# Kernel tuning notes

Hardware: AMD Instinct MI355X
Metric: run time of the kernel (lower is better)

## Reference

```python
import jax, jax.numpy as jnp
import numpy as np

N = 100000   # nodes
E = 1600000  # edges (avg degree 16)
F = 128      # input features
H = 64       # hidden_dim
C = 10       # num_classes
G = 128      # graphs in batch
EPS = 1e-5   # BatchNorm eps


def setup_inputs() -> dict:
    key = jax.random.key(0)
    ks = jax.random.split(key, 24)
    d = {}
    d['x'] = jax.random.normal(ks[0], (N, F), jnp.float32)
    d['edge_index'] = jax.random.randint(ks[1], (2, E), 0, N)
    d['batch'] = jnp.sort(jax.random.randint(ks[2], (N,), 0, G))
    # SAGEConv1: lin_l (aggregated, with bias) + lin_r (root, no bias)
    d['W1l'] = jax.random.normal(ks[3], (F, H), jnp.float32) * 0.05
    d['W1r'] = jax.random.normal(ks[4], (F, H), jnp.float32) * 0.05
    d['b1'] = jnp.zeros((H,), jnp.float32)
    # SAGEConv2
    d['W2l'] = jax.random.normal(ks[5], (H, H), jnp.float32) * 0.1
    d['W2r'] = jax.random.normal(ks[6], (H, H), jnp.float32) * 0.1
    d['b2'] = jnp.zeros((H,), jnp.float32)
    # BatchNorm (eval mode: running stats)
    for i, (kg, kb, km, kv) in enumerate([(7, 8, 9, 10), (11, 12, 13, 14), (15, 16, 17, 18)], 1):
        d[f'bn{i}_g'] = jax.random.uniform(ks[kg], (H,), jnp.float32, 0.5, 1.5)
        d[f'bn{i}_b'] = jax.random.normal(ks[kb], (H,), jnp.float32) * 0.1
        d[f'bn{i}_m'] = jax.random.normal(ks[km], (H,), jnp.float32) * 0.1
        d[f'bn{i}_v'] = jax.random.uniform(ks[kv], (H,), jnp.float32, 0.5, 1.5)
    # classifier head
    d['Wc1'] = jax.random.normal(ks[19], (H, H), jnp.float32) * 0.1
    d['bc1'] = jnp.zeros((H,), jnp.float32)
    d['Wc2'] = jax.random.normal(ks[20], (H, C), jnp.float32) * 0.1
    d['bc2'] = jnp.zeros((C,), jnp.float32)
    return d


def _bn(x, g, b, m, v):
    return (x - m) * jax.lax.rsqrt(v + EPS) * g + b


def _sage(x, src, dst, Wl, Wr, b):
    # mean aggregation of source-node features at destination nodes
    msum = jax.ops.segment_sum(x[src], dst, num_segments=N)          # [N, d]
    cnt = jax.ops.segment_sum(jnp.ones((E,), x.dtype), dst, num_segments=N)
    mean = msum / jnp.maximum(cnt, 1.0)[:, None]
    return mean @ Wl + b + x @ Wr


def reference(x, edge_index, batch,
              W1l, W1r, b1, W2l, W2r, b2,
              bn1_g, bn1_b, bn1_m, bn1_v,
              bn2_g, bn2_b, bn2_m, bn2_v,
              Wc1, bc1, bn3_g, bn3_b, bn3_m, bn3_v,
              Wc2, bc2):
    src, dst = edge_index[0], edge_index[1]
    h = _sage(x, src, dst, W1l, W1r, b1)
    h = jax.nn.relu(_bn(h, bn1_g, bn1_b, bn1_m, bn1_v))
    h = _sage(h, src, dst, W2l, W2r, b2)
    h = jax.nn.relu(_bn(h, bn2_g, bn2_b, bn2_m, bn2_v))
    # global mean pool over graphs
    gsum = jax.ops.segment_sum(h, batch, num_segments=G)             # [G, H]
    gcnt = jax.ops.segment_sum(jnp.ones((N,), h.dtype), batch, num_segments=G)
    g = gsum / jnp.maximum(gcnt, 1.0)[:, None]
    # classifier head (eval: dropout is identity)
    g = jax.nn.relu(_bn(g @ Wc1 + bc1, bn3_g, bn3_b, bn3_m, bn3_v))
    logits = g @ Wc2 + bc2
    return jax.nn.log_softmax(logits, axis=1)
```

## Files before the change

kernel.cpp:

```cpp
#include <hip/hip_runtime.h>
#include <hip/hip_bf16.h>
#include <math.h>

#define NN 100000
#define NE 1600000
#define FF 128
#define HH 64
#define CC 10
#define GG 128
#define BN_EPS 1e-5f

#define BNODES 64
#define NB 1563
#define PBLK 256
#define ECHUNK 6250
#define SCOL_CAP 2048

#define PNODES 16
#define POOL_BLOCKS 1563

typedef short v8bf __attribute__((ext_vector_type(8)));
typedef float v4f  __attribute__((ext_vector_type(4)));

__device__ inline ushort f2b(float x) {
    __hip_bfloat16 h = __float2bfloat16(x);
    return *reinterpret_cast<ushort*>(&h);
}
__device__ inline float b2f(ushort u) {
    return __uint_as_float(((unsigned)u) << 16);
}
__device__ inline float blo(unsigned u) { return __uint_as_float(u << 16); }
__device__ inline float bhi(unsigned u) { return __uint_as_float(u & 0xffff0000u); }

__device__ inline void sw_one(const float* __restrict__ W, ushort* __restrict__ o,
                              int t, int K) {
    const int lane = t & 63, nt = (t >> 6) & 3, ks = t >> 8;
    const int m = lane & 15, quad = lane >> 4;
#pragma unroll
    for (int j = 0; j < 8; ++j) {
        const int kk = ks * 32 + quad * 8 + j;
        const int cc = nt * 16 + m;
        o[t * 8 + j] = f2b(W[kk * 64 + cc]);
    }
}

__global__ __launch_bounds__(256) void prep_kernel(const float* __restrict__ W1l,
                                                   const float* __restrict__ W1r,
                                                   const float* __restrict__ W2l,
                                                   const float* __restrict__ W2r,
                                                   ushort* __restrict__ w1ls,
                                                   ushort* __restrict__ w1rs,
                                                   ushort* __restrict__ w2ls,
                                                   ushort* __restrict__ w2rs,
                                                   float* __restrict__ gz) {
    const int t = blockIdx.x * 256 + threadIdx.x;
    if (t < 1024) {
        sw_one(W1l, w1ls, t, FF);
        sw_one(W1r, w1rs, t, FF);
    } else if (t < 1536) {
        sw_one(W2l, w2ls, t - 1024, HH);
        sw_one(W2r, w2rs, t - 1024, HH);
    } else {
        for (int i = t - 1536; i < GG * 64 + GG; i += 512) gz[i] = 0.f;
    }
}

template<int K, int TPB, bool AF32>
__global__ __launch_bounds__(256) void gemm_mfma(const void* __restrict__ Xv,
                                                 const ushort* __restrict__ Bl,
                                                 const ushort* __restrict__ Br,
                                                 ushort* __restrict__ Yl,
                                                 ushort* __restrict__ Yr) {
    constexpr int KS = K / 32;
    const int lane  = threadIdx.x & 63;
    const int wave  = threadIdx.x >> 6;
    const int nhalf = wave & 1;
    const int rsub  = wave >> 1;
    const int m = lane & 15, quad = lane >> 4;

    v8bf bl[KS][2], br[KS][2];
#pragma unroll
    for (int ks = 0; ks < KS; ++ks)
#pragma unroll
        for (int nt = 0; nt < 2; ++nt) {
            const int nti = nhalf * 2 + nt;
            bl[ks][nt] = *(const v8bf*)(Bl + ((size_t)(ks * 4 + nti) * 64 + lane) * 8);
            br[ks][nt] = *(const v8bf*)(Br + ((size_t)(ks * 4 + nti) * 64 + lane) * 8);
        }

    for (int it = 0; it < TPB; ++it) {
        const int bt = blockIdx.x * TPB + it;
        const int row0 = bt * 32 + rsub * 16;
        if (row0 >= NN) return;
        const v4f z = {0.f, 0.f, 0.f, 0.f};
        v4f accl[2] = {z, z}, accr[2] = {z, z};
#pragma unroll
        for (int ks = 0; ks < KS; ++ks) {
            v8bf a;
            if (AF32) {
                const float* xrow = (const float*)Xv + (size_t)(row0 + m) * K + quad * 8 + ks * 32;
                const float4 a0 = *(const float4*)(xrow);
                const float4 a1 = *(const float4*)(xrow + 4);
                a[0] = (short)f2b(a0.x); a[1] = (short)f2b(a0.y);
                a[2] = (short)f2b(a0.z); a[3] = (short)f2b(a0.w);
                a[4] = (short)f2b(a1.x); a[5] = (short)f2b(a1.y);
                a[6] = (short)f2b(a1.z); a[7] = (short)f2b(a1.w);
            } else {
                const ushort* xrow = (const ushort*)Xv + (size_t)(row0 + m) * K + quad * 8 + ks * 32;
                a = *(const v8bf*)xrow;
            }
#pragma unroll
            for (int nt = 0; nt < 2; ++nt) {
                accl[nt] = __builtin_amdgcn_mfma_f32_16x16x32_bf16(a, bl[ks][nt], accl[nt], 0, 0, 0);
                accr[nt] = __builtin_amdgcn_mfma_f32_16x16x32_bf16(a, br[ks][nt], accr[nt], 0, 0, 0);
            }
        }
#pragma unroll
        for (int nt = 0; nt < 2; ++nt) {
            const int cc = nhalf * 32 + nt * 16 + m;
#pragma unroll
            for (int r = 0; r < 4; ++r) {
                const size_t off = (size_t)(row0 + quad * 4 + r) * 64 + cc;
                Yl[off] = f2b(accl[nt][r]);
                Yr[off] = f2b(accr[nt][r]);
            }
        }
    }
}

__global__ __launch_bounds__(1024) void edge_sort(const int* __restrict__ src,
                                                  const int* __restrict__ dst,
                                                  int* __restrict__ lofs,
                                                  int* __restrict__ pairs) {
    __shared__ int lcnt[NB];
    __shared__ int lpos[NB];
    __shared__ int psum[1024];
    const int tid = threadIdx.x;
    const int b = blockIdx.x;
    const int e0 = b * ECHUNK;

    for (int i = tid; i < NB; i += 1024) lcnt[i] = 0;
    __syncthreads();
    for (int e = e0 + tid; e < e0 + ECHUNK; e += 1024)
        atomicAdd(&lcnt[dst[e] >> 6], 1);
    __syncthreads();

    const int i0 = 2 * tid, i1 = 2 * tid + 1;
    const int v0 = (i0 < NB) ? lcnt[i0] : 0;
    const int v1 = (i1 < NB) ? lcnt[i1] : 0;
    psum[tid] = v0 + v1;
    __syncthreads();
    for (int off = 1; off < 1024; off <<= 1) {
        int t = (tid >= off) ? psum[tid - off] : 0;
        __syncthreads();
        psum[tid] += t;
        __syncthreads();
    }
    const int base = psum[tid] - v0 - v1;
    if (i0 < NB) lpos[i0] = base;
    if (i1 < NB) lpos[i1] = base + v0;
    __syncthreads();

    for (int i = tid; i < NB; i += 1024) lofs[(size_t)b * NB + i] = lpos[i];
    for (int i = tid; i < NB; i += 1024) lcnt[i] = lpos[i];
    __syncthreads();

    for (int e = e0 + tid; e < e0 + ECHUNK; e += 1024) {
        const int s = src[e];
        const int d = dst[e];
        const int pos = atomicAdd(&lcnt[d >> 6], 1);
        pairs[e0 + pos] = (s << 6) | (d & (BNODES - 1));
    }
}

__global__ __launch_bounds__(256) void spmm_sorted(const int* __restrict__ lofs,
                                                   const int* __restrict__ pairs,
                                                   const ushort* __restrict__ Yl,
                                                   const ushort* __restrict__ Yr,
                                                   const float* __restrict__ bias,
                                                   const float* __restrict__ bng,
                                                   const float* __restrict__ bnb,
                                                   const float* __restrict__ bnm,
                                                   const float* __restrict__ bnv,
                                                   ushort* __restrict__ outp) {
    __shared__ int scol2[SCOL_CAP];
    __shared__ int scol[SCOL_CAP];
    __shared__ int deg[BNODES];
    __shared__ int loffs[BNODES];
    __shared__ int fill[BNODES];
    __shared__ int rbs[256];
    __shared__ int total_s;
    const int tid = threadIdx.x;
    const int b = blockIdx.x;

    if (tid < BNODES) { deg[tid] = 0; fill[tid] = 0; }

    const int lo = lofs[(size_t)tid * NB + b];
    const int hi = (b == NB - 1) ? ECHUNK : lofs[(size_t)tid * NB + b + 1];
    int len = hi - lo;
    rbs[tid] = len;
    __syncthreads();
    for (int off = 1; off < 256; off <<= 1) {
        int t = (tid >= off) ? rbs[tid - off] : 0;
        __syncthreads();
        rbs[tid] += t;
        __syncthreads();
    }
    int rbase = rbs[tid] - len;
    if (tid == 255) total_s = (rbs[255] > SCOL_CAP) ? SCOL_CAP : rbs[255];
    if (rbase >= SCOL_CAP) len = 0;
    else if (rbase + len > SCOL_CAP) len = SCOL_CAP - rbase;

    const int gbase = tid * ECHUNK + lo;
    for (int j = 0; j < len; ++j) {
        const int v = pairs[gbase + j];
        scol2[rbase + j] = v;
        atomicAdd(&deg[v & (BNODES - 1)], 1);
    }
    __syncthreads();
    const int total = total_s;

    if (tid < BNODES) loffs[tid] = deg[tid];
    __syncthreads();
    for (int s = 1; s < BNODES; s <<= 1) {
        int v = 0;
        if (tid < BNODES && tid >= s) v = loffs[tid - s];
        __syncthreads();
        if (tid < BNODES) loffs[tid] += v;
        __syncthreads();
    }

    for (int j = tid; j < total; j += 256) {
        const int v = scol2[j];
        const int dl = v & (BNODES - 1);
        const int pos = (loffs[dl] - deg[dl]) + atomicAdd(&fill[dl], 1);
        scol[pos] = v >> 6;
    }
    __syncthreads();

    const int wv = tid >> 6, lane = tid & 63;
    const int grp = lane >> 3, subl = lane & 7;

    float biasj[8], scj[8], mj[8], bbj[8];
#pragma unroll
    for (int j = 0; j < 8; ++j) {
        const int ch = subl * 8 + j;
        biasj[j] = bias[ch];
        scj[j] = bng[ch] * rsqrtf(bnv[ch] + BN_EPS);
        mj[j] = bnm[ch];
        bbj[j] = bnb[ch];
    }

    for (int i = 0; i < 2; ++i) {
        const int nl = wv * 16 + i * 8 + grp;
        const int node = b * BNODES + nl;
        if (node >= NN) continue;
        const int dg = deg[nl];
        const int nbeg = loffs[nl] - dg;
        const int nend = nbeg + dg;
        float a[8] = {0.f, 0.f, 0.f, 0.f, 0.f, 0.f, 0.f, 0.f};
        float c[8] = {0.f, 0.f, 0.f, 0.f, 0.f, 0.f, 0.f, 0.f};
        int e = nbeg;
        for (; e + 1 < nend; e += 2) {
            const int s0 = scol[e];
            const int s1 = scol[e + 1];
            const uint4 r0 = *(const uint4*)(Yl + (size_t)s0 * 64 + subl * 8);
            const uint4 r1 = *(const uint4*)(Yl + (size_t)s1 * 64 + subl * 8);
            a[0] += blo(r0.x); a[1] += bhi(r0.x); a[2] += blo(r0.y); a[3] += bhi(r0.y);
            a[4] += blo(r0.z); a[5] += bhi(r0.z); a[6] += blo(r0.w); a[7] += bhi(r0.w);
            c[0] += blo(r1.x); c[1] += bhi(r1.x); c[2] += blo(r1.y); c[3] += bhi(r1.y);
            c[4] += blo(r1.z); c[5] += bhi(r1.z); c[6] += blo(r1.w); c[7] += bhi(r1.w);
        }
        if (e < nend) {
            const int s0 = scol[e];
            const uint4 r0 = *(const uint4*)(Yl + (size_t)s0 * 64 + subl * 8);
            a[0] += blo(r0.x); a[1] += bhi(r0.x); a[2] += blo(r0.y); a[3] += bhi(r0.y);
            a[4] += blo(r0.z); a[5] += bhi(r0.z); a[6] += blo(r0.w); a[7] += bhi(r0.w);
        }
        const float inv = 1.0f / fmaxf((float)dg, 1.0f);
        const uint4 yr = *(const uint4*)(Yr + (size_t)node * 64 + subl * 8);
        float hj[8];
        hj[0] = (a[0] + c[0]) * inv + biasj[0] + blo(yr.x);
        hj[1] = (a[1] + c[1]) * inv + biasj[1] + bhi(yr.x);
        hj[2] = (a[2] + c[2]) * inv + biasj[2] + blo(yr.y);
        hj[3] = (a[3] + c[3]) * inv + biasj[3] + bhi(yr.y);
        hj[4] = (a[4] + c[4]) * inv + biasj[4] + blo(yr.z);
        hj[5] = (a[5] + c[5]) * inv + biasj[5] + bhi(yr.z);
        hj[6] = (a[6] + c[6]) * inv + biasj[6] + blo(yr.w);
        hj[7] = (a[7] + c[7]) * inv + biasj[7] + bhi(yr.w);
        unsigned ow[4];
#pragma unroll
        for (int j = 0; j < 4; ++j) {
            const float o0 = fmaxf((hj[2 * j] - mj[2 * j]) * scj[2 * j] + bbj[2 * j], 0.0f);
            const float o1 = fmaxf((hj[2 * j + 1] - mj[2 * j + 1]) * scj[2 * j + 1] + bbj[2 * j + 1], 0.0f);
            ow[j] = (unsigned)f2b(o0) | ((unsigned)f2b(o1) << 16);
        }
        uint4 o;
        o.x = ow[0]; o.y = ow[1]; o.z = ow[2]; o.w = ow[3];
        *(uint4*)(outp + (size_t)node * 64 + subl * 8) = o;
    }
}

__global__ __launch_bounds__(256) void pool_seg(const ushort* __restrict__ h,
                                                const int* __restrict__ batch,
                                                float* __restrict__ gsum,
                                                float* __restrict__ gcnt) {
    const int wave = blockIdx.x * 4 + (threadIdx.x >> 6);
    const int lane = threadIdx.x & 63;
    const int n0 = wave * PNODES;
    if (n0 >= NN) return;
    const int n1 = (n0 + PNODES < NN) ? n0 + PNODES : NN;
    int g = batch[n0];
    float acc = 0.f, c = 0.f;
#pragma unroll 4
    for (int n = n0; n < n1; ++n) {
        const int b = batch[n];
        if (b != g) {
            atomicAdd(&gsum[g * 64 + lane], acc);
            if (lane == 0) atomicAdd(&gcnt[g], c);
            acc = 0.f; c = 0.f; g = b;
        }
        acc += b2f(h[(size_t)n * 64 + lane]);
        c += 1.0f;
    }
    atomicAdd(&gsum[g * 64 + lane], acc);
    if (lane == 0) atomicAdd(&gcnt[g], c);
}

__global__ __launch_bounds__(64) void head_kernel(const float* __restrict__ gsum,
                                                  const float* __restrict__ gcnt,
                                                  const float* __restrict__ Wc1,
                                                  const float* __restrict__ bc1,
                                                  const float* __restrict__ g3,
                                                  const float* __restrict__ b3,
                                                  const float* __restrict__ m3,
                                                  const float* __restrict__ v3,
                                                  const float* __restrict__ Wc2,
                                                  const float* __restrict__ bc2,
                                                  float* __restrict__ out) {
    __shared__ float sg[64];
    __shared__ float st[64];
    __shared__ float sl[10];
    __shared__ float sls;
    const int b = blockIdx.x;
    const int c = threadIdx.x;
    sg[c] = gsum[b * 64 + c] / fmaxf(gcnt[b], 1.0f);
    __syncthreads();
    float acc = bc1[c];
#pragma unroll
    for (int k = 0; k < 64; ++k) acc += sg[k] * Wc1[k * 64 + c];
    const float sc = g3[c] * rsqrtf(v3[c] + BN_EPS);
    st[c] = fmaxf((acc - m3[c]) * sc + b3[c], 0.0f);
    __syncthreads();
    if (c < CC) {
        float lg = bc2[c];
#pragma unroll
        for (int k = 0; k < 64; ++k) lg += st[k] * Wc2[k * CC + c];
        sl[c] = lg;
    }
    __syncthreads();
    if (c == 0) {
        float mx = sl[0];
        for (int i = 1; i < CC; ++i) mx = fmaxf(mx, sl[i]);
        float s = 0.f;
        for (int i = 0; i < CC; ++i) s += expf(sl[i] - mx);
        sls = mx + logf(s);
    }
    __syncthreads();
    if (c < CC) out[b * CC + c] = sl[c] - sls;
}

extern "C" void kernel_launch(void* const* d_in, const int* in_sizes, int n_in,
                              void* d_out, int out_size, void* d_ws, size_t ws_size,
                              hipStream_t stream) {
    const float* x    = (const float*)d_in[0];
    const int*   ei   = (const int*)d_in[1];
    const int*   batch= (const int*)d_in[2];
    const float* W1l  = (const float*)d_in[3];
    const float* W1r  = (const float*)d_in[4];
    const float* b1   = (const float*)d_in[5];
    const float* W2l  = (const float*)d_in[6];
    const float* W2r  = (const float*)d_in[7];
    const float* b2   = (const float*)d_in[8];
    const float* bn1g = (const float*)d_in[9];
    const float* bn1b = (const float*)d_in[10];
    const float* bn1m = (const float*)d_in[11];
    const float* bn1v = (const float*)d_in[12];
    const float* bn2g = (const float*)d_in[13];
    const float* bn2b = (const float*)d_in[14];
    const float* bn2m = (const float*)d_in[15];
    const float* bn2v = (const float*)d_in[16];
    const float* bn3g = (const float*)d_in[17];
    const float* bn3b = (const float*)d_in[18];
    const float* bn3m = (const float*)d_in[19];
    const float* bn3v = (const float*)d_in[20];
    const float* Wc1  = (const float*)d_in[21];
    const float* bc1  = (const float*)d_in[22];
    const float* Wc2  = (const float*)d_in[23];
    const float* bc2  = (const float*)d_in[24];
    float* out = (float*)d_out;

    const int* src = ei;
    const int* dst = ei + NE;

    char* p = (char*)d_ws;
    ushort* yl   = (ushort*)p;                 p += (size_t)NN * 64 * 2;
    ushort* yr   = (ushort*)p;                 p += (size_t)NN * 64 * 2;
    ushort* hbuf = (ushort*)p;                 p += (size_t)NN * 64 * 2;
    int*    pairs= (int*)p;                    p += (size_t)NE * 4;
    int*    lofs = (int*)p;                    p += (size_t)PBLK * NB * 4;
    ushort* w1ls = (ushort*)p;                 p += (size_t)FF * 64 * 2;
    ushort* w1rs = (ushort*)p;                 p += (size_t)FF * 64 * 2;
    ushort* w2ls = (ushort*)p;                 p += (size_t)HH * 64 * 2;
    ushort* w2rs = (ushort*)p;                 p += (size_t)HH * 64 * 2;
    float* gsum  = (float*)p;                  p += (size_t)GG * 64 * 4;
    float* gcnt  = gsum + GG * 64;             p += (size_t)GG * 4;

    edge_sort<<<PBLK, 1024, 0, stream>>>(src, dst, lofs, pairs);

    prep_kernel<<<8, 256, 0, stream>>>(W1l, W1r, W2l, W2r, w1ls, w1rs, w2ls, w2rs, gsum);

    gemm_mfma<FF, 2, true><<<1563, 256, 0, stream>>>((const void*)x, w1ls, w1rs, yl, yr);
    spmm_sorted<<<NB, 256, 0, stream>>>(lofs, pairs, yl, yr, b1,
                                        bn1g, bn1b, bn1m, bn1v, hbuf);

    gemm_mfma<HH, 2, false><<<1563, 256, 0, stream>>>((const void*)hbuf, w2ls, w2rs, yl, yr);
    spmm_sorted<<<NB, 256, 0, stream>>>(lofs, pairs, yl, yr, b2,
                                        bn2g, bn2b, bn2m, bn2v, hbuf);

    pool_seg<<<POOL_BLOCKS, 256, 0, stream>>>(hbuf, batch, gsum, gcnt);
    head_kernel<<<GG, 64, 0, stream>>>(gsum, gcnt, Wc1, bc1,
                                       bn3g, bn3b, bn3m, bn3v, Wc2, bc2, out);
}
```

Before: 317.8 us.

## Build a global bucket-sorted edge list so SpMM reads contiguous ranges

Replaces the per-chunk local sort, where each SpMM block gathered 256 scattered slices through a strided offsets table and a 256-step scan, with a global counting sort. A histogram kernel counts edges per bucket, a one-block scan computes global bucket bases, and the write kernel stages each chunk in LDS and then scatters it into globally contiguous bucket ranges. SpMM blocks then read one contiguous range, with coalesced loads and no offset scan or staging buffer. This adds two extra launches and a memset, uses global atomics for bucket cursors so order within a bucket is nondeterministic, and silently drops entries if a block handles more than 8 edges per thread.

```diff
diff --git a/kernel.cpp b/kernel.cpp
--- a/kernel.cpp
+++ b/kernel.cpp
@@ -128,16 +128,53 @@
     }
 }
 
-__global__ __launch_bounds__(1024) void edge_sort(const int* __restrict__ src,
-                                                  const int* __restrict__ dst,
-                                                  int* __restrict__ lofs,
-                                                  int* __restrict__ pairs) {
+__global__ __launch_bounds__(1024) void edge_hist(const int* __restrict__ dst,
+                                                  int* __restrict__ btot) {
+    __shared__ int h[NB];
+    for (int i = threadIdx.x; i < NB; i += 1024) h[i] = 0;
+    __syncthreads();
+    const int e0 = blockIdx.x * ECHUNK;
+    for (int e = e0 + threadIdx.x; e < e0 + ECHUNK; e += 1024)
+        atomicAdd(&h[dst[e] >> 6], 1);
+    __syncthreads();
+    for (int i = threadIdx.x; i < NB; i += 1024)
+        if (h[i]) atomicAdd(&btot[i], h[i]);
+}
+
+__global__ __launch_bounds__(1024) void scan_buckets(const int* __restrict__ btot,
+                                                     int* __restrict__ bbase) {
+    __shared__ int psum[1024];
+    const int tid = threadIdx.x;
+    const int i0 = 2 * tid, i1 = 2 * tid + 1;
+    const int v0 = (i0 < NB) ? btot[i0] : 0;
+    const int v1 = (i1 < NB) ? btot[i1] : 0;
+    psum[tid] = v0 + v1;
+    __syncthreads();
+    for (int off = 1; off < 1024; off <<= 1) {
+        int t = (tid >= off) ? psum[tid - off] : 0;
+        __syncthreads();
+        psum[tid] += t;
+        __syncthreads();
+    }
+    const int base = psum[tid] - v0 - v1;
+    if (i0 < NB) bbase[i0] = base;
+    if (i1 < NB) bbase[i1] = base + v0;
+    if (tid == 0) bbase[NB] = NE;
+}
+
+__global__ __launch_bounds__(1024) void edge_sort_write(const int* __restrict__ src,
+                                                        const int* __restrict__ dst,
+                                                        const int* __restrict__ bbase,
+                                                        int* __restrict__ bcur,
+                                                        int* __restrict__ pairs) {
     __shared__ int lcnt[NB];
     __shared__ int lpos[NB];
+    __shared__ int gdelta[NB];
     __shared__ int psum[1024];
+    __shared__ int sval[ECHUNK];
+    __shared__ short sbkt[ECHUNK];
     const int tid = threadIdx.x;
-    const int b = blockIdx.x;
-    const int e0 = b * ECHUNK;
+    const int e0 = blockIdx.x * ECHUNK;
 
     for (int i = tid; i < NB; i += 1024) lcnt[i] = 0;
     __syncthreads();
@@ -161,19 +198,30 @@
     if (i1 < NB) lpos[i1] = base + v0;
     __syncthreads();
 
-    for (int i = tid; i < NB; i += 1024) lofs[(size_t)b * NB + i] = lpos[i];
+    for (int i = tid; i < NB; i += 1024) {
+        const int len = lcnt[i];
+        const int rb = len ? atomicAdd(&bcur[i], len) : 0;
+        gdelta[i] = bbase[i] + rb - lpos[i];
+    }
+    __syncthreads();
     for (int i = tid; i < NB; i += 1024) lcnt[i] = lpos[i];
     __syncthreads();
 
     for (int e = e0 + tid; e < e0 + ECHUNK; e += 1024) {
         const int s = src[e];
         const int d = dst[e];
-        const int pos = atomicAdd(&lcnt[d >> 6], 1);
-        pairs[e0 + pos] = (s << 6) | (d & (BNODES - 1));
-    }
-}
-
-__global__ __launch_bounds__(256) void spmm_sorted(const int* __restrict__ lofs,
+        const int b = d >> 6;
+        const int p = atomicAdd(&lcnt[b], 1);
+        sval[p] = (s << 6) | (d & (BNODES - 1));
+        sbkt[p] = (short)b;
+    }
+    __syncthreads();
+
+    for (int j = tid; j < ECHUNK; j += 1024)
+        pairs[j + gdelta[sbkt[j]]] = sval[j];
+}
+
+__global__ __launch_bounds__(256) void spmm_sorted(const int* __restrict__ bbase,
                                                    const int* __restrict__ pairs,
                                                    const ushort* __restrict__ Yl,
                                                    const ushort* __restrict__ Yr,
@@ -183,42 +231,28 @@
                                                    const float* __restrict__ bnm,
                                                    const float* __restrict__ bnv,
                                                    ushort* __restrict__ outp) {
-    __shared__ int scol2[SCOL_CAP];
     __shared__ int scol[SCOL_CAP];
     __shared__ int deg[BNODES];
     __shared__ int loffs[BNODES];
     __shared__ int fill[BNODES];
-    __shared__ int rbs[256];
-    __shared__ int total_s;
     const int tid = threadIdx.x;
     const int b = blockIdx.x;
 
     if (tid < BNODES) { deg[tid] = 0; fill[tid] = 0; }
-
-    const int lo = lofs[(size_t)tid * NB + b];
-    const int hi = (b == NB - 1) ? ECHUNK : lofs[(size_t)tid * NB + b + 1];
-    int len = hi - lo;
-    rbs[tid] = len;
-    __syncthreads();
-    for (int off = 1; off < 256; off <<= 1) {
-        int t = (tid >= off) ? rbs[tid - off] : 0;
-        __syncthreads();
-        rbs[tid] += t;
-        __syncthreads();
-    }
-    int rbase = rbs[tid] - len;
-    if (tid == 255) total_s = (rbs[255] > SCOL_CAP) ? SCOL_CAP : rbs[255];
-    if (rbase >= SCOL_CAP) len = 0;
-    else if (rbase + len > SCOL_CAP) len = SCOL_CAP - rbase;
-
-    const int gbase = tid * ECHUNK + lo;
-    for (int j = 0; j < len; ++j) {
-        const int v = pairs[gbase + j];
-        scol2[rbase + j] = v;
+    __syncthreads();
+
+    const int beg = bbase[b];
+    int end = bbase[b + 1];
+    if (end - beg > SCOL_CAP) end = beg + SCOL_CAP;
+
+    int pv[8];
+    int npv = 0;
+    for (int i = beg + tid; i < end; i += 256) {
+        const int v = pairs[i];
+        pv[npv++] = v;
         atomicAdd(&deg[v & (BNODES - 1)], 1);
     }
     __syncthreads();
-    const int total = total_s;
 
     if (tid < BNODES) loffs[tid] = deg[tid];
     __syncthreads();
@@ -230,8 +264,8 @@
         __syncthreads();
     }
 
-    for (int j = tid; j < total; j += 256) {
-        const int v = scol2[j];
+    for (int j = 0; j < npv; ++j) {
+        const int v = pv[j];
         const int dl = v & (BNODES - 1);
         const int pos = (loffs[dl] - deg[dl]) + atomicAdd(&fill[dl], 1);
         scol[pos] = v >> 6;
@@ -408,7 +442,9 @@
     ushort* yr   = (ushort*)p;                 p += (size_t)NN * 64 * 2;
     ushort* hbuf = (ushort*)p;                 p += (size_t)NN * 64 * 2;
     int*    pairs= (int*)p;                    p += (size_t)NE * 4;
-    int*    lofs = (int*)p;                    p += (size_t)PBLK * NB * 4;
+    int*    btot = (int*)p;                    p += (size_t)NB * 4;
+    int*    bcur = (int*)p;                    p += (size_t)NB * 4;
+    int*    bbase= (int*)p;                    p += (size_t)(NB + 1) * 4;
     ushort* w1ls = (ushort*)p;                 p += (size_t)FF * 64 * 2;
     ushort* w1rs = (ushort*)p;                 p += (size_t)FF * 64 * 2;
     ushort* w2ls = (ushort*)p;                 p += (size_t)HH * 64 * 2;
@@ -416,16 +452,19 @@
     float* gsum  = (float*)p;                  p += (size_t)GG * 64 * 4;
     float* gcnt  = gsum + GG * 64;             p += (size_t)GG * 4;
 
-    edge_sort<<<PBLK, 1024, 0, stream>>>(src, dst, lofs, pairs);
+    hipMemsetAsync(btot, 0, (size_t)2 * NB * sizeof(int), stream);
+    edge_hist<<<PBLK, 1024, 0, stream>>>(dst, btot);
+    scan_buckets<<<1, 1024, 0, stream>>>(btot, bbase);
+    edge_sort_write<<<PBLK, 1024, 0, stream>>>(src, dst, bbase, bcur, pairs);
 
     prep_kernel<<<8, 256, 0, stream>>>(W1l, W1r, W2l, W2r, w1ls, w1rs, w2ls, w2rs, gsum);
 
     gemm_mfma<FF, 2, true><<<1563, 256, 0, stream>>>((const void*)x, w1ls, w1rs, yl, yr);
-    spmm_sorted<<<NB, 256, 0, stream>>>(lofs, pairs, yl, yr, b1,
+    spmm_sorted<<<NB, 256, 0, stream>>>(bbase, pairs, yl, yr, b1,
                                         bn1g, bn1b, bn1m, bn1v, hbuf);
 
     gemm_mfma<HH, 2, false><<<1563, 256, 0, stream>>>((const void*)hbuf, w2ls, w2rs, yl, yr);
-    spmm_sorted<<<NB, 256, 0, stream>>>(lofs, pairs, yl, yr, b2,
+    spmm_sorted<<<NB, 256, 0, stream>>>(bbase, pairs, yl, yr, b2,
                                         bn2g, bn2b, bn2m, bn2v, hbuf);
 
     pool_seg<<<POOL_BLOCKS, 256, 0, stream>>>(hbuf, batch, gsum, gcnt);
```

New measurement: 294.9 us. 7.2% less time.
